# Kernel tuning notes

Measured on AMD Instinct MI355X. Metric: run time of the kernel, lower is better.

The kernel has to match this reference:

```python
import jax, jax.numpy as jnp
import numpy as np

BETA = 0.5  # exp-sum normalization exponent (not a true softmax)


def setup_inputs() -> dict:
    key = jax.random.key(0)
    ks = jax.random.split(key, 12)
    b, h = 1024, 200
    item_num, region_num, user_num = 50000, 1000, 10000
    d, hid = 128, 128  # embed_size == hidden_size (required by the bmm reshape)
    std = 0.01
    return {
        "history": jax.random.randint(ks[0], (1, b, h), 0, item_num),
        "target": jax.random.randint(ks[1], (1, b), 0, item_num),
        "history_region": jax.random.randint(ks[2], (1, b, h), 0, region_num),
        "target_region": jax.random.randint(ks[3], (1, b), 0, region_num),
        "history_visit_rate": jax.random.uniform(ks[4], (1, h), dtype=jnp.float32),
        "dist_mat": jax.random.uniform(ks[5], (b, h), dtype=jnp.float32),
        "uid": 7,
        "embed_target": std * jax.random.normal(ks[6], (item_num, d // 2), dtype=jnp.float32),
        "embed_region": std * jax.random.normal(ks[7], (region_num, d // 2), dtype=jnp.float32),
        "embed_dist": std * jax.random.normal(ks[8], (user_num, region_num), dtype=jnp.float32),
        "Wq": jax.random.normal(ks[9], (hid, d), dtype=jnp.float32) * (1.0 / np.sqrt(d)),
        "Wk": jax.random.normal(ks[10], (hid, d), dtype=jnp.float32) * (1.0 / np.sqrt(d)),
        "Wv": jax.random.normal(ks[11], (d, d), dtype=jnp.float32) * (1.0 / np.sqrt(d)),
    }


def reference(history, target, history_region, target_region, history_visit_rate,
              dist_mat, uid, embed_target, embed_region, embed_dist, Wq, Wk, Wv):
    h_idx = history[0]            # [b, h]
    tgt = target[0]               # [b]
    hr = history_region[0]        # [b, h]
    tr = target_region[0]         # [b]
    hv = history_visit_rate[0]    # [h]
    b, hlen = h_idx.shape

    # embedding gathers + concat (target half | region half)
    hist_emb = jnp.concatenate([embed_target[h_idx], embed_region[hr]], axis=-1)  # [b,h,d]
    tgt_emb = jnp.concatenate([embed_target[tgt], embed_region[tr]], axis=-1)     # [b,d]
    hd = embed_dist[uid][hr]      # [b, h]
    td = embed_dist[uid][tr]      # [b]
    d = tgt_emb.shape[1]

    # QKV projections (torch Linear: y = x @ W.T)
    q = tgt_emb @ Wq.T            # [b, d]  (hidden == d)
    k = hist_emb @ Wk.T           # [b, h, d]
    v = hist_emb @ Wv.T           # [b, h, d]

    # faithful to original: key reshaped (NOT transposed) to [b, d, h]
    k_r = k.reshape(b, d, hlen)
    scores = jnp.einsum('bd,bdh->bh', q, k_r) / jnp.sqrt(jnp.float32(d))  # [b,h]

    # exp / beta-normalized attention with equality mask
    mask = (h_idx != tgt[:, None]).astype(scores.dtype)
    exp_A = jnp.exp(scores) * mask                          # [b,h]
    exp_sum = jnp.sum(exp_A, axis=-1) ** BETA               # [b]
    attn = exp_A / exp_sum[:, None]                         # [b,h]

    # geo weights: td @ hd is a vector-matrix product -> [h], broadcast over b
    geo = jnp.exp(-1.0 / (jax.nn.relu(td @ hd) + 1.0) * dist_mat)  # [b,h]

    result1 = v * (attn + geo)[..., None]                   # [b,h,d]
    result2 = hist_emb * jnp.broadcast_to(hv, (b, hlen))[..., None]
    result = result1 + result2                              # [b,h,d]

    pred = jnp.einsum('bhd,bd->b', result, tgt_emb)         # bmm + sum over h
    return jax.nn.sigmoid(pred)
```

## Files before the change

### kernel.cpp

```cpp
#include <hip/hip_runtime.h>

typedef unsigned short USH;
typedef unsigned int   UIN;

static constexpr int Bn = 1024;
static constexpr int Hn = 200;
static constexpr int Dn = 128;
static constexpr int Dh = 64;
static constexpr int NITEM = 50000;
static constexpr int NREG  = 1000;
static constexpr int MT = 64;
static constexpr int AB_A_BLOCKS = (NITEM + MT - 1) / MT;
static constexpr int AB_B_BLOCKS = (NREG  + MT - 1) / MT;
static constexpr int WTS = 132;
static constexpr int ETS = 69;
static constexpr int CR = 50;

__device__ __forceinline__ float bf2f(USH u) {
  return __uint_as_float(((UIN)u) << 16);
}
__device__ __forceinline__ float2 pb2f2(UIN p) {
  float2 r;
  r.x = __uint_as_float(p << 16);
  r.y = __uint_as_float(p & 0xffff0000u);
  return r;
}
__device__ __forceinline__ USH f2b(float f) {
  UIN x = __float_as_uint(f);
  return (USH)((x + 0x7fffu + ((x >> 16) & 1u)) >> 16);
}
__device__ __forceinline__ UIN addpk(UIN u, UIN v) {
  float2 a = pb2f2(u), b = pb2f2(v);
  return (UIN)f2b(a.x + b.x) | ((UIN)f2b(a.y + b.y) << 16);
}

__global__ __launch_bounds__(256) void g_kernel(
    const int* __restrict__ hregion, const int* __restrict__ tregion,
    const float* __restrict__ embed_dist, const int* __restrict__ uid,
    float* __restrict__ g) {
  int c = threadIdx.x;
  const float* row = embed_dist + (size_t)uid[0] * NREG;
  float acc = 0.f;
  int ibase = blockIdx.x * 16;
  for (int ii = 0; ii < 16; ii++) {
    int i = ibase + ii;
    float td = row[tregion[i]];
    if (c < Hn) acc += td * row[hregion[(size_t)i * Hn + c]];
  }
  if (c < Hn) atomicAdd(&g[c], acc);
}

__global__ __launch_bounds__(256, 2) void ab_kernel(
    const float* __restrict__ Et, const float* __restrict__ Er,
    const float* __restrict__ Wk, USH* __restrict__ A, USH* __restrict__ Bt,
    USH* __restrict__ Ebr, USH* __restrict__ Err, int emit_raw) {
  __shared__ float wt[64 * WTS];
  __shared__ float et[MT * ETS];
  int blk = blockIdx.x, tid = threadIdx.x;
  const float* E; USH* Out; USH* OutR; int nmax, base, koff;
  if (blk < AB_A_BLOCKS) { E = Et; Out = A;  OutR = Ebr; nmax = NITEM; base = blk * MT; koff = 0; }
  else { E = Er; Out = Bt; OutR = Err; nmax = NREG; base = (blk - AB_A_BLOCKS) * MT; koff = 64; }

#pragma unroll
  for (int p = 0; p < 8; p++) {
    int idx = p * 256 + tid;
    int row = idx >> 4, c4 = idx & 15;
    float4 w = *reinterpret_cast<const float4*>(Wk + (size_t)row * Dn + koff + c4 * 4);
    wt[(c4 * 4 + 0) * WTS + row] = w.x;
    wt[(c4 * 4 + 1) * WTS + row] = w.y;
    wt[(c4 * 4 + 2) * WTS + row] = w.z;
    wt[(c4 * 4 + 3) * WTS + row] = w.w;
  }
#pragma unroll
  for (int p = 0; p < 4; p++) {
    int idx = p * 256 + tid;
    int m = idx >> 4, c4 = idx & 15;
    int gi = base + m;
    float4 e = make_float4(0.f, 0.f, 0.f, 0.f);
    if (gi < nmax) e = *reinterpret_cast<const float4*>(E + (size_t)gi * Dh + c4 * 4);
    et[m * ETS + c4 * 4 + 0] = e.x;
    et[m * ETS + c4 * 4 + 1] = e.y;
    et[m * ETS + c4 * 4 + 2] = e.z;
    et[m * ETS + c4 * 4 + 3] = e.w;
  }
  __syncthreads();

  if (emit_raw) {
#pragma unroll
    for (int q = 0; q < 8; q++) {
      int idx = q * 256 + tid;
      int m = idx >> 5, kp = idx & 31;
      int gi = base + m;
      if (gi < nmax) {
        UIN pk = (UIN)f2b(et[m * ETS + 2 * kp]) | ((UIN)f2b(et[m * ETS + 2 * kp + 1]) << 16);
        *reinterpret_cast<UIN*>(OutR + (size_t)gi * Dh + 2 * kp) = pk;
      }
    }
  }

  int jt = tid & 15, it = tid >> 4;
  const float* wb = wt + jt * 8;
  const float* eb = et + (it * 4) * ETS;
  float c[4][8];
#pragma unroll
  for (int ii = 0; ii < 4; ii++)
#pragma unroll
    for (int jj = 0; jj < 8; jj++) c[ii][jj] = 0.f;

#pragma unroll 2
  for (int k = 0; k < 64; k++) {
    float4 w0 = *reinterpret_cast<const float4*>(wb + (size_t)k * WTS);
    float4 w1 = *reinterpret_cast<const float4*>(wb + (size_t)k * WTS + 4);
    float e0 = eb[k], e1 = eb[ETS + k], e2 = eb[2 * ETS + k], e3 = eb[3 * ETS + k];
    c[0][0] += e0 * w0.x; c[0][1] += e0 * w0.y; c[0][2] += e0 * w0.z; c[0][3] += e0 * w0.w;
    c[0][4] += e0 * w1.x; c[0][5] += e0 * w1.y; c[0][6] += e0 * w1.z; c[0][7] += e0 * w1.w;
    c[1][0] += e1 * w0.x; c[1][1] += e1 * w0.y; c[1][2] += e1 * w0.z; c[1][3] += e1 * w0.w;
    c[1][4] += e1 * w1.x; c[1][5] += e1 * w1.y; c[1][6] += e1 * w1.z; c[1][7] += e1 * w1.w;
    c[2][0] += e2 * w0.x; c[2][1] += e2 * w0.y; c[2][2] += e2 * w0.z; c[2][3] += e2 * w0.w;
    c[2][4] += e2 * w1.x; c[2][5] += e2 * w1.y; c[2][6] += e2 * w1.z; c[2][7] += e2 * w1.w;
    c[3][0] += e3 * w0.x; c[3][1] += e3 * w0.y; c[3][2] += e3 * w0.z; c[3][3] += e3 * w0.w;
    c[3][4] += e3 * w1.x; c[3][5] += e3 * w1.y; c[3][6] += e3 * w1.z; c[3][7] += e3 * w1.w;
  }

#pragma unroll
  for (int ii = 0; ii < 4; ii++) {
    int item = base + it * 4 + ii;
    if (item < nmax) {
      uint4 pk;
      pk.x = (UIN)f2b(c[ii][0]) | ((UIN)f2b(c[ii][1]) << 16);
      pk.y = (UIN)f2b(c[ii][2]) | ((UIN)f2b(c[ii][3]) << 16);
      pk.z = (UIN)f2b(c[ii][4]) | ((UIN)f2b(c[ii][5]) << 16);
      pk.w = (UIN)f2b(c[ii][6]) | ((UIN)f2b(c[ii][7]) << 16);
      *reinterpret_cast<uint4*>(Out + (size_t)item * Dn + jt * 8) = pk;
    }
  }
}

__global__ __launch_bounds__(256, 4) void sc_kernel(
    const int* __restrict__ history, const int* __restrict__ target,
    const int* __restrict__ hregion, const int* __restrict__ tregion,
    const float* __restrict__ Et, const float* __restrict__ Er,
    const float* __restrict__ Wq, const USH* __restrict__ A,
    const USH* __restrict__ Bt, float* __restrict__ psc) {
  __shared__ USH kvs[CR * Dn];
  __shared__ float tgtE[128], qp[128], qv[32];
  int b = blockIdx.x, i = b >> 2, h = b & 3;
  int tid = threadIdx.x;
  const int* hrow = history + (size_t)i * Hn + CR * h;
  const int* rrow = hregion + (size_t)i * Hn + CR * h;

  if (tid < 64)       tgtE[tid] = Et[(size_t)target[i] * Dh + tid];
  else if (tid < 128) tgtE[tid] = Er[(size_t)tregion[i] * Dh + (tid - 64)];

  int rlane = tid & 15, rgrp = tid >> 4;
#pragma unroll
  for (int p = 0; p < 4; p++) {
    int t = p * 16 + rgrp;
    if (t < CR) {
      int ia = hrow[t], ib = rrow[t];
      uint4 av = *reinterpret_cast<const uint4*>(A  + (size_t)ia * Dn + rlane * 8);
      uint4 bv = *reinterpret_cast<const uint4*>(Bt + (size_t)ib * Dn + rlane * 8);
      uint4 pk;
      pk.x = addpk(av.x, bv.x); pk.y = addpk(av.y, bv.y);
      pk.z = addpk(av.z, bv.z); pk.w = addpk(av.w, bv.w);
      *reinterpret_cast<uint4*>(&kvs[t * Dn + rlane * 8]) = pk;
    }
  }
  __syncthreads();

  if (tid < 128) {
    int ql = tid >> 2, quarter = tid & 3;
    int a = 32 * h + ql;
    const float4* wp = reinterpret_cast<const float4*>(Wq + (size_t)a * Dn + quarter * 32);
    float acc = 0.f;
#pragma unroll
    for (int k4 = 0; k4 < 8; k4++) {
      float4 w = wp[k4];
      const float* tv = &tgtE[quarter * 32 + k4 * 4];
      acc += w.x * tv[0] + w.y * tv[1] + w.z * tv[2] + w.w * tv[3];
    }
    qp[tid] = acc;
  }
  __syncthreads();
  if (tid < 32)
    qv[tid] = (qp[4 * tid] + qp[4 * tid + 1] + qp[4 * tid + 2] + qp[4 * tid + 3])
              * 0.088388347648318447f;
  __syncthreads();

  if (tid < Hn) {
    float acc = 0.f;
    const USH* kp = &kvs[tid];
#pragma unroll
    for (int a = 0; a < 32; a++) acc += qv[a] * bf2f(kp[a * 200]);
    psc[((size_t)i * 4 + h) * Hn + tid] = acc;
  }
}

__global__ __launch_bounds__(256, 4) void ep_kernel(
    const int* __restrict__ history, const int* __restrict__ target,
    const int* __restrict__ hregion, const int* __restrict__ tregion,
    const float* __restrict__ hv, const float* __restrict__ dist_mat,
    const float* __restrict__ Et, const float* __restrict__ Er,
    const float* __restrict__ Wv, const float* __restrict__ g,
    const USH* __restrict__ Ebr, const USH* __restrict__ Err,
    const float* __restrict__ psc, int use_raw, float* __restrict__ out) {
  __shared__ float tgtE[128], uv[128], red[8];
  int i = blockIdx.x, tid = threadIdx.x, lane = tid & 63, wave = tid >> 6;
  int tgt_i = target[i], tr_i = tregion[i];
  const int* hrow = history + (size_t)i * Hn;
  const int* rrow = hregion + (size_t)i * Hn;

  if (tid < 64)       tgtE[tid] = Et[(size_t)tgt_i * Dh + tid];
  else if (tid < 128) tgtE[tid] = Er[(size_t)tr_i * Dh + (tid - 64)];
  __syncthreads();

  if (tid >= 128) {
    int d = tid - 128;
    float a0 = 0.f, a1 = 0.f, a2 = 0.f, a3 = 0.f;
#pragma unroll 8
    for (int j = 0; j < 128; j += 4) {
      a0 += Wv[(size_t)(j + 0) * Dn + d] * tgtE[j + 0];
      a1 += Wv[(size_t)(j + 1) * Dn + d] * tgtE[j + 1];
      a2 += Wv[(size_t)(j + 2) * Dn + d] * tgtE[j + 2];
      a3 += Wv[(size_t)(j + 3) * Dn + d] * tgtE[j + 3];
    }
    uv[d] = (a0 + a1) + (a2 + a3);
  }
  __syncthreads();

  float ea = 0.f, sc1 = 0.f, sc2 = 0.f;
  if (tid < Hn) {
    const float* pp = psc + (size_t)i * 4 * Hn + tid;
    float s = (pp[0] + pp[Hn]) + (pp[2 * Hn] + pp[3 * Hn]);
    int ia2 = hrow[tid], ib2 = rrow[tid];
    float p1 = 0.f, p2 = 0.f;
    if (use_raw) {
      const uint4* epu = reinterpret_cast<const uint4*>(Ebr + (size_t)ia2 * Dh);
      const uint4* rpu = reinterpret_cast<const uint4*>(Err + (size_t)ib2 * Dh);
#pragma unroll
      for (int k8 = 0; k8 < 8; k8++) {
        uint4 e = epu[k8], r = rpu[k8];
        float2 e0 = pb2f2(e.x), e1 = pb2f2(e.y), e2 = pb2f2(e.z), e3 = pb2f2(e.w);
        float2 r0 = pb2f2(r.x), r1 = pb2f2(r.y), r2 = pb2f2(r.z), r3 = pb2f2(r.w);
        const float* u0 = &uv[k8 * 8];       const float* t0 = &tgtE[k8 * 8];
        const float* u1 = &uv[64 + k8 * 8];  const float* t1 = &tgtE[64 + k8 * 8];
        p1 += e0.x * u0[0] + e0.y * u0[1] + e1.x * u0[2] + e1.y * u0[3]
            + e2.x * u0[4] + e2.y * u0[5] + e3.x * u0[6] + e3.y * u0[7]
            + r0.x * u1[0] + r0.y * u1[1] + r1.x * u1[2] + r1.y * u1[3]
            + r2.x * u1[4] + r2.y * u1[5] + r3.x * u1[6] + r3.y * u1[7];
        p2 += e0.x * t0[0] + e0.y * t0[1] + e1.x * t0[2] + e1.y * t0[3]
            + e2.x * t0[4] + e2.y * t0[5] + e3.x * t0[6] + e3.y * t0[7]
            + r0.x * t1[0] + r0.y * t1[1] + r1.x * t1[2] + r1.y * t1[3]
            + r2.x * t1[4] + r2.y * t1[5] + r3.x * t1[6] + r3.y * t1[7];
      }
    } else {
      const float4* ep = reinterpret_cast<const float4*>(Et + (size_t)ia2 * Dh);
      const float4* rp = reinterpret_cast<const float4*>(Er + (size_t)ib2 * Dh);
#pragma unroll
      for (int k4 = 0; k4 < 16; k4++) {
        float4 e = ep[k4], r = rp[k4];
        const float* u0 = &uv[k4 * 4];        const float* t0 = &tgtE[k4 * 4];
        const float* u1 = &uv[64 + k4 * 4];   const float* t1 = &tgtE[64 + k4 * 4];
        p1 += e.x * u0[0] + e.y * u0[1] + e.z * u0[2] + e.w * u0[3]
            + r.x * u1[0] + r.y * u1[1] + r.z * u1[2] + r.w * u1[3];
        p2 += e.x * t0[0] + e.y * t0[1] + e.z * t0[2] + e.w * t0[3]
            + r.x * t1[0] + r.y * t1[1] + r.z * t1[2] + r.w * t1[3];
      }
    }
    sc1 = p1; sc2 = p2;
    ea = (ia2 != tgt_i) ? __expf(s) : 0.f;
  }

  float wsum = ea;
  for (int off = 32; off > 0; off >>= 1) wsum += __shfl_down(wsum, off, 64);
  if (lane == 0) red[wave] = wsum;
  __syncthreads();
  float esum = red[0] + red[1] + red[2] + red[3];
  float inv = esum > 0.f ? 1.f / sqrtf(esum) : 0.f;

  float part = 0.f;
  if (tid < Hn) {
    float attn = ea * inv;
    float gc = g[tid]; gc = gc > 0.f ? gc : 0.f;
    float dm = dist_mat[(size_t)i * Hn + tid];
    float geo = __expf(-dm / (gc + 1.f));
    part = (attn + geo) * sc1 + hv[tid] * sc2;
  }
  __syncthreads();
  for (int off = 32; off > 0; off >>= 1) part += __shfl_down(part, off, 64);
  if (lane == 0) red[wave] = part;
  __syncthreads();
  if (tid == 0) {
    float pred = red[0] + red[1] + red[2] + red[3];
    out[i] = 1.f / (1.f + __expf(-pred));
  }
}

extern "C" void kernel_launch(void* const* d_in, const int* in_sizes, int n_in,
                              void* d_out, int out_size, void* d_ws, size_t ws_size,
                              hipStream_t stream) {
  const int*   history = (const int*)d_in[0];
  const int*   target  = (const int*)d_in[1];
  const int*   hregion = (const int*)d_in[2];
  const int*   tregion = (const int*)d_in[3];
  const float* hv      = (const float*)d_in[4];
  const float* dist    = (const float*)d_in[5];
  const int*   uid     = (const int*)d_in[6];
  const float* Et      = (const float*)d_in[7];
  const float* Er      = (const float*)d_in[8];
  const float* Edist   = (const float*)d_in[9];
  const float* Wq      = (const float*)d_in[10];
  const float* Wk      = (const float*)d_in[11];
  const float* Wv      = (const float*)d_in[12];

  float* g = (float*)d_ws;
  USH* A   = (USH*)((char*)d_ws + 1024);
  USH* Bt  = A + (size_t)NITEM * Dn;
  USH* Ebr = Bt + (size_t)NREG * Dn;
  USH* Err = Ebr + (size_t)NITEM * Dh;
  float* psc = (float*)(Err + (size_t)NREG * Dh);
  size_t need_raw = 1024 + 2 * ((size_t)NITEM * Dn + (size_t)NREG * Dn +
                                (size_t)NITEM * Dh + (size_t)NREG * Dh) +
                    4 * (size_t)Bn * 4 * Hn;
  int use_raw = (ws_size >= need_raw) ? 1 : 0;
  float* out = (float*)d_out;

  hipMemsetAsync(g, 0, Hn * sizeof(float), stream);
  g_kernel<<<Bn / 16, 256, 0, stream>>>(hregion, tregion, Edist, uid, g);
  ab_kernel<<<AB_A_BLOCKS + AB_B_BLOCKS, 256, 0, stream>>>(Et, Er, Wk, A, Bt,
                                                           Ebr, Err, use_raw);
  sc_kernel<<<Bn * 4, 256, 0, stream>>>(history, target, hregion, tregion,
                                        Et, Er, Wq, A, Bt, psc);
  ep_kernel<<<Bn, 256, 0, stream>>>(history, target, hregion, tregion, hv, dist,
                                    Et, Er, Wv, g, Ebr, Err, psc, use_raw, out);
}
```

Measured before the change: 172.7 us.

## Interleave projected and raw embeddings, precompute q/u vectors, move dot products into sc_kernel

Projected-key rows and raw bf16 embeddings are stored interleaved in a single 192-wide row per item, so sc_kernel's gathers hit adjacent memory. The per-batch Wq and Wv target projections move into extra blocks of ab_kernel and are written to global memory, so they are no longer recomputed in every sc and ep block. The history-embedding dot products against u and the target embedding move from ep_kernel into sc_kernel, reusing the same gathered rows and leaving ep_kernel as a light reduction. This costs more workspace, extra global round-trips for qvt, uvt and s12, and drops the fp32 fallback path when the workspace is small.

Measured after the change: 160.2 us. 7.3% less time.

```diff
diff --git a/kernel.cpp b/kernel.cpp
--- a/kernel.cpp
+++ b/kernel.cpp
@@ -12,9 +12,12 @@
 static constexpr int MT = 64;
 static constexpr int AB_A_BLOCKS = (NITEM + MT - 1) / MT;
 static constexpr int AB_B_BLOCKS = (NREG  + MT - 1) / MT;
+static constexpr int AB_TOT = AB_A_BLOCKS + AB_B_BLOCKS;
+static constexpr int QU_BLOCKS = Bn / 4;
 static constexpr int WTS = 132;
 static constexpr int ETS = 69;
-static constexpr int CR = 50;
+static constexpr int CR  = 50;
+static constexpr int AFS = 192;
 
 __device__ __forceinline__ float bf2f(USH u) {
   return __uint_as_float(((UIN)u) << 16);
@@ -52,14 +55,61 @@
 
 __global__ __launch_bounds__(256, 2) void ab_kernel(
     const float* __restrict__ Et, const float* __restrict__ Er,
-    const float* __restrict__ Wk, USH* __restrict__ A, USH* __restrict__ Bt,
-    USH* __restrict__ Ebr, USH* __restrict__ Err, int emit_raw) {
+    const float* __restrict__ Wk, const float* __restrict__ Wq,
+    const float* __restrict__ Wv, const int* __restrict__ target,
+    const int* __restrict__ tregion,
+    USH* __restrict__ Af, USH* __restrict__ Bf,
+    float* __restrict__ qvt, float* __restrict__ uvt) {
   __shared__ float wt[64 * WTS];
   __shared__ float et[MT * ETS];
   int blk = blockIdx.x, tid = threadIdx.x;
-  const float* E; USH* Out; USH* OutR; int nmax, base, koff;
-  if (blk < AB_A_BLOCKS) { E = Et; Out = A;  OutR = Ebr; nmax = NITEM; base = blk * MT; koff = 0; }
-  else { E = Er; Out = Bt; OutR = Err; nmax = NREG; base = (blk - AB_A_BLOCKS) * MT; koff = 64; }
+
+  if (blk >= AB_TOT) {
+    float* te = wt;
+    int i0 = (blk - AB_TOT) * 4;
+#pragma unroll
+    for (int v = 0; v < 2; v++) {
+      int idx = v * 256 + tid;
+      int ii = idx >> 7, d = idx & 127;
+      int it = i0 + ii;
+      te[ii * 128 + d] = (d < 64) ? Et[(size_t)target[it] * Dh + d]
+                                  : Er[(size_t)tregion[it] * Dh + (d - 64)];
+    }
+    __syncthreads();
+    int j = tid & 127, half = tid >> 7;
+    float a0 = 0.f, a1 = 0.f, a2 = 0.f, a3 = 0.f;
+    if (half == 0) {
+      const float* wr = Wq + (size_t)j * Dn;
+#pragma unroll 8
+      for (int k = 0; k < 128; k++) {
+        float w = wr[k];
+        a0 += w * te[k]; a1 += w * te[128 + k];
+        a2 += w * te[256 + k]; a3 += w * te[384 + k];
+      }
+      const float s = 0.088388347648318447f;
+      qvt[(size_t)(i0 + 0) * Dn + j] = a0 * s;
+      qvt[(size_t)(i0 + 1) * Dn + j] = a1 * s;
+      qvt[(size_t)(i0 + 2) * Dn + j] = a2 * s;
+      qvt[(size_t)(i0 + 3) * Dn + j] = a3 * s;
+    } else {
+      int d = j;
+#pragma unroll 8
+      for (int k = 0; k < 128; k++) {
+        float w = Wv[(size_t)k * Dn + d];
+        a0 += w * te[k]; a1 += w * te[128 + k];
+        a2 += w * te[256 + k]; a3 += w * te[384 + k];
+      }
+      uvt[(size_t)(i0 + 0) * Dn + d] = a0;
+      uvt[(size_t)(i0 + 1) * Dn + d] = a1;
+      uvt[(size_t)(i0 + 2) * Dn + d] = a2;
+      uvt[(size_t)(i0 + 3) * Dn + d] = a3;
+    }
+    return;
+  }
+
+  const float* E; USH* Out; int nmax, base, koff;
+  if (blk < AB_A_BLOCKS) { E = Et; Out = Af; nmax = NITEM; base = blk * MT; koff = 0; }
+  else { E = Er; Out = Bf; nmax = NREG; base = (blk - AB_A_BLOCKS) * MT; koff = 64; }
 
 #pragma unroll
   for (int p = 0; p < 8; p++) {
@@ -85,16 +135,14 @@
   }
   __syncthreads();
 
-  if (emit_raw) {
-#pragma unroll
-    for (int q = 0; q < 8; q++) {
-      int idx = q * 256 + tid;
-      int m = idx >> 5, kp = idx & 31;
-      int gi = base + m;
-      if (gi < nmax) {
-        UIN pk = (UIN)f2b(et[m * ETS + 2 * kp]) | ((UIN)f2b(et[m * ETS + 2 * kp + 1]) << 16);
-        *reinterpret_cast<UIN*>(OutR + (size_t)gi * Dh + 2 * kp) = pk;
-      }
+#pragma unroll
+  for (int q = 0; q < 8; q++) {
+    int idx = q * 256 + tid;
+    int m = idx >> 5, kp = idx & 31;
+    int gi = base + m;
+    if (gi < nmax) {
+      UIN pk = (UIN)f2b(et[m * ETS + 2 * kp]) | ((UIN)f2b(et[m * ETS + 2 * kp + 1]) << 16);
+      *reinterpret_cast<UIN*>(Out + (size_t)gi * AFS + 128 + 2 * kp) = pk;
     }
   }
 
@@ -131,7 +179,7 @@
       pk.y = (UIN)f2b(c[ii][2]) | ((UIN)f2b(c[ii][3]) << 16);
       pk.z = (UIN)f2b(c[ii][4]) | ((UIN)f2b(c[ii][5]) << 16);
       pk.w = (UIN)f2b(c[ii][6]) | ((UIN)f2b(c[ii][7]) << 16);
-      *reinterpret_cast<uint4*>(Out + (size_t)item * Dn + jt * 8) = pk;
+      *reinterpret_cast<uint4*>(Out + (size_t)item * AFS + jt * 8) = pk;
     }
   }
 }
@@ -140,52 +188,70 @@
     const int* __restrict__ history, const int* __restrict__ target,
     const int* __restrict__ hregion, const int* __restrict__ tregion,
     const float* __restrict__ Et, const float* __restrict__ Er,
-    const float* __restrict__ Wq, const USH* __restrict__ A,
-    const USH* __restrict__ Bt, float* __restrict__ psc) {
+    const float* __restrict__ qvt, const float* __restrict__ uvt,
+    const USH* __restrict__ Af, const USH* __restrict__ Bf,
+    float* __restrict__ psc, float2* __restrict__ s12) {
   __shared__ USH kvs[CR * Dn];
-  __shared__ float tgtE[128], qp[128], qv[32];
+  __shared__ float tgtE[128], uvf[128], qv[32];
   int b = blockIdx.x, i = b >> 2, h = b & 3;
   int tid = threadIdx.x;
   const int* hrow = history + (size_t)i * Hn + CR * h;
   const int* rrow = hregion + (size_t)i * Hn + CR * h;
 
-  if (tid < 64)       tgtE[tid] = Et[(size_t)target[i] * Dh + tid];
-  else if (tid < 128) tgtE[tid] = Er[(size_t)tregion[i] * Dh + (tid - 64)];
-
-  int rlane = tid & 15, rgrp = tid >> 4;
-#pragma unroll
-  for (int p = 0; p < 4; p++) {
-    int t = p * 16 + rgrp;
-    if (t < CR) {
-      int ia = hrow[t], ib = rrow[t];
-      uint4 av = *reinterpret_cast<const uint4*>(A  + (size_t)ia * Dn + rlane * 8);
-      uint4 bv = *reinterpret_cast<const uint4*>(Bt + (size_t)ib * Dn + rlane * 8);
-      uint4 pk;
-      pk.x = addpk(av.x, bv.x); pk.y = addpk(av.y, bv.y);
-      pk.z = addpk(av.z, bv.z); pk.w = addpk(av.w, bv.w);
-      *reinterpret_cast<uint4*>(&kvs[t * Dn + rlane * 8]) = pk;
-    }
-  }
-  __syncthreads();
-
   if (tid < 128) {
-    int ql = tid >> 2, quarter = tid & 3;
-    int a = 32 * h + ql;
-    const float4* wp = reinterpret_cast<const float4*>(Wq + (size_t)a * Dn + quarter * 32);
-    float acc = 0.f;
-#pragma unroll
-    for (int k4 = 0; k4 < 8; k4++) {
-      float4 w = wp[k4];
-      const float* tv = &tgtE[quarter * 32 + k4 * 4];
-      acc += w.x * tv[0] + w.y * tv[1] + w.z * tv[2] + w.w * tv[3];
-    }
-    qp[tid] = acc;
-  }
-  __syncthreads();
-  if (tid < 32)
-    qv[tid] = (qp[4 * tid] + qp[4 * tid + 1] + qp[4 * tid + 2] + qp[4 * tid + 3])
-              * 0.088388347648318447f;
-  __syncthreads();
+    tgtE[tid] = (tid < 64) ? Et[(size_t)target[i] * Dh + tid]
+                           : Er[(size_t)tregion[i] * Dh + (tid - 64)];
+  } else {
+    uvf[tid - 128] = uvt[(size_t)i * Dn + (tid - 128)];
+  }
+  if (tid < 32) qv[tid] = qvt[(size_t)i * Dn + 32 * h + tid];
+
+  {
+    int rlane = tid & 15, rgrp = tid >> 4;
+#pragma unroll
+    for (int p = 0; p < 4; p++) {
+      int t = p * 16 + rgrp;
+      if (t < CR) {
+        int ia = hrow[t], ib = rrow[t];
+        uint4 av = *reinterpret_cast<const uint4*>(Af + (size_t)ia * AFS + rlane * 8);
+        uint4 bv = *reinterpret_cast<const uint4*>(Bf + (size_t)ib * AFS + rlane * 8);
+        uint4 pk;
+        pk.x = addpk(av.x, bv.x); pk.y = addpk(av.y, bv.y);
+        pk.z = addpk(av.z, bv.z); pk.w = addpk(av.w, bv.w);
+        *reinterpret_cast<uint4*>(&kvs[t * Dn + rlane * 8]) = pk;
+      }
+    }
+  }
+  __syncthreads();
+
+  {
+    int l8 = tid & 7, r8 = tid >> 3;
+#pragma unroll
+    for (int p = 0; p < 2; p++) {
+      int t = p * 32 + r8;
+      if (t < CR) {
+        int ia = hrow[t], ib = rrow[t];
+        uint4 e = *reinterpret_cast<const uint4*>(Af + (size_t)ia * AFS + 128 + l8 * 8);
+        uint4 r = *reinterpret_cast<const uint4*>(Bf + (size_t)ib * AFS + 128 + l8 * 8);
+        float2 e0 = pb2f2(e.x), e1 = pb2f2(e.y), e2 = pb2f2(e.z), e3 = pb2f2(e.w);
+        float2 r0 = pb2f2(r.x), r1 = pb2f2(r.y), r2 = pb2f2(r.z), r3 = pb2f2(r.w);
+        const float* u0 = &uvf[l8 * 8];       const float* t0 = &tgtE[l8 * 8];
+        const float* u1 = &uvf[64 + l8 * 8];  const float* t1 = &tgtE[64 + l8 * 8];
+        float s1a = e0.x * u0[0] + e0.y * u0[1] + e1.x * u0[2] + e1.y * u0[3]
+                  + e2.x * u0[4] + e2.y * u0[5] + e3.x * u0[6] + e3.y * u0[7]
+                  + r0.x * u1[0] + r0.y * u1[1] + r1.x * u1[2] + r1.y * u1[3]
+                  + r2.x * u1[4] + r2.y * u1[5] + r3.x * u1[6] + r3.y * u1[7];
+        float s2a = e0.x * t0[0] + e0.y * t0[1] + e1.x * t0[2] + e1.y * t0[3]
+                  + e2.x * t0[4] + e2.y * t0[5] + e3.x * t0[6] + e3.y * t0[7]
+                  + r0.x * t1[0] + r0.y * t1[1] + r1.x * t1[2] + r1.y * t1[3]
+                  + r2.x * t1[4] + r2.y * t1[5] + r3.x * t1[6] + r3.y * t1[7];
+        s1a += __shfl_xor(s1a, 1, 64); s2a += __shfl_xor(s2a, 1, 64);
+        s1a += __shfl_xor(s1a, 2, 64); s2a += __shfl_xor(s2a, 2, 64);
+        s1a += __shfl_xor(s1a, 4, 64); s2a += __shfl_xor(s2a, 4, 64);
+        if (l8 == 0) s12[(size_t)i * Hn + CR * h + t] = make_float2(s1a, s2a);
+      }
+    }
+  }
 
   if (tid < Hn) {
     float acc = 0.f;
@@ -196,81 +262,22 @@
   }
 }
 
-__global__ __launch_bounds__(256, 4) void ep_kernel(
+__global__ __launch_bounds__(256, 8) void ep_kernel(
     const int* __restrict__ history, const int* __restrict__ target,
-    const int* __restrict__ hregion, const int* __restrict__ tregion,
     const float* __restrict__ hv, const float* __restrict__ dist_mat,
-    const float* __restrict__ Et, const float* __restrict__ Er,
-    const float* __restrict__ Wv, const float* __restrict__ g,
-    const USH* __restrict__ Ebr, const USH* __restrict__ Err,
-    const float* __restrict__ psc, int use_raw, float* __restrict__ out) {
-  __shared__ float tgtE[128], uv[128], red[8];
+    const float* __restrict__ g, const float* __restrict__ psc,
+    const float2* __restrict__ s12, float* __restrict__ out) {
+  __shared__ float red[8];
   int i = blockIdx.x, tid = threadIdx.x, lane = tid & 63, wave = tid >> 6;
-  int tgt_i = target[i], tr_i = tregion[i];
-  const int* hrow = history + (size_t)i * Hn;
-  const int* rrow = hregion + (size_t)i * Hn;
-
-  if (tid < 64)       tgtE[tid] = Et[(size_t)tgt_i * Dh + tid];
-  else if (tid < 128) tgtE[tid] = Er[(size_t)tr_i * Dh + (tid - 64)];
-  __syncthreads();
-
-  if (tid >= 128) {
-    int d = tid - 128;
-    float a0 = 0.f, a1 = 0.f, a2 = 0.f, a3 = 0.f;
-#pragma unroll 8
-    for (int j = 0; j < 128; j += 4) {
-      a0 += Wv[(size_t)(j + 0) * Dn + d] * tgtE[j + 0];
-      a1 += Wv[(size_t)(j + 1) * Dn + d] * tgtE[j + 1];
-      a2 += Wv[(size_t)(j + 2) * Dn + d] * tgtE[j + 2];
-      a3 += Wv[(size_t)(j + 3) * Dn + d] * tgtE[j + 3];
-    }
-    uv[d] = (a0 + a1) + (a2 + a3);
-  }
-  __syncthreads();
-
-  float ea = 0.f, sc1 = 0.f, sc2 = 0.f;
+  int tgt_i = target[i];
+
+  float ea = 0.f; float2 sv = make_float2(0.f, 0.f);
   if (tid < Hn) {
     const float* pp = psc + (size_t)i * 4 * Hn + tid;
     float s = (pp[0] + pp[Hn]) + (pp[2 * Hn] + pp[3 * Hn]);
-    int ia2 = hrow[tid], ib2 = rrow[tid];
-    float p1 = 0.f, p2 = 0.f;
-    if (use_raw) {
-      const uint4* epu = reinterpret_cast<const uint4*>(Ebr + (size_t)ia2 * Dh);
-      const uint4* rpu = reinterpret_cast<const uint4*>(Err + (size_t)ib2 * Dh);
-#pragma unroll
-      for (int k8 = 0; k8 < 8; k8++) {
-        uint4 e = epu[k8], r = rpu[k8];
-        float2 e0 = pb2f2(e.x), e1 = pb2f2(e.y), e2 = pb2f2(e.z), e3 = pb2f2(e.w);
-        float2 r0 = pb2f2(r.x), r1 = pb2f2(r.y), r2 = pb2f2(r.z), r3 = pb2f2(r.w);
-        const float* u0 = &uv[k8 * 8];       const float* t0 = &tgtE[k8 * 8];
-        const float* u1 = &uv[64 + k8 * 8];  const float* t1 = &tgtE[64 + k8 * 8];
-        p1 += e0.x * u0[0] + e0.y * u0[1] + e1.x * u0[2] + e1.y * u0[3]
-            + e2.x * u0[4] + e2.y * u0[5] + e3.x * u0[6] + e3.y * u0[7]
-            + r0.x * u1[0] + r0.y * u1[1] + r1.x * u1[2] + r1.y * u1[3]
-            + r2.x * u1[4] + r2.y * u1[5] + r3.x * u1[6] + r3.y * u1[7];
-        p2 += e0.x * t0[0] + e0.y * t0[1] + e1.x * t0[2] + e1.y * t0[3]
-            + e2.x * t0[4] + e2.y * t0[5] + e3.x * t0[6] + e3.y * t0[7]
-            + r0.x * t1[0] + r0.y * t1[1] + r1.x * t1[2] + r1.y * t1[3]
-            + r2.x * t1[4] + r2.y * t1[5] + r3.x * t1[6] + r3.y * t1[7];
-      }
-    } else {
-      const float4* ep = reinterpret_cast<const float4*>(Et + (size_t)ia2 * Dh);
-      const float4* rp = reinterpret_cast<const float4*>(Er + (size_t)ib2 * Dh);
-#pragma unroll
-      for (int k4 = 0; k4 < 16; k4++) {
-        float4 e = ep[k4], r = rp[k4];
-        const float* u0 = &uv[k4 * 4];        const float* t0 = &tgtE[k4 * 4];
-        const float* u1 = &uv[64 + k4 * 4];   const float* t1 = &tgtE[64 + k4 * 4];
-        p1 += e.x * u0[0] + e.y * u0[1] + e.z * u0[2] + e.w * u0[3]
-            + r.x * u1[0] + r.y * u1[1] + r.z * u1[2] + r.w * u1[3];
-        p2 += e.x * t0[0] + e.y * t0[1] + e.z * t0[2] + e.w * t0[3]
-            + r.x * t1[0] + r.y * t1[1] + r.z * t1[2] + r.w * t1[3];
-      }
-    }
-    sc1 = p1; sc2 = p2;
-    ea = (ia2 != tgt_i) ? __expf(s) : 0.f;
-  }
-
+    sv = s12[(size_t)i * Hn + tid];
+    ea = (history[(size_t)i * Hn + tid] != tgt_i) ? __expf(s) : 0.f;
+  }
   float wsum = ea;
   for (int off = 32; off > 0; off >>= 1) wsum += __shfl_down(wsum, off, 64);
   if (lane == 0) red[wave] = wsum;
@@ -280,11 +287,10 @@
 
   float part = 0.f;
   if (tid < Hn) {
-    float attn = ea * inv;
     float gc = g[tid]; gc = gc > 0.f ? gc : 0.f;
     float dm = dist_mat[(size_t)i * Hn + tid];
     float geo = __expf(-dm / (gc + 1.f));
-    part = (attn + geo) * sc1 + hv[tid] * sc2;
+    part = (ea * inv + geo) * sv.x + hv[tid] * sv.y;
   }
   __syncthreads();
   for (int off = 32; off > 0; off >>= 1) part += __shfl_down(part, off, 64);
@@ -313,24 +319,21 @@
   const float* Wk      = (const float*)d_in[11];
   const float* Wv      = (const float*)d_in[12];
 
-  float* g = (float*)d_ws;
-  USH* A   = (USH*)((char*)d_ws + 1024);
-  USH* Bt  = A + (size_t)NITEM * Dn;
-  USH* Ebr = Bt + (size_t)NREG * Dn;
-  USH* Err = Ebr + (size_t)NITEM * Dh;
-  float* psc = (float*)(Err + (size_t)NREG * Dh);
-  size_t need_raw = 1024 + 2 * ((size_t)NITEM * Dn + (size_t)NREG * Dn +
-                                (size_t)NITEM * Dh + (size_t)NREG * Dh) +
-                    4 * (size_t)Bn * 4 * Hn;
-  int use_raw = (ws_size >= need_raw) ? 1 : 0;
+  char* w = (char*)d_ws;
+  float* g   = (float*)w;
+  USH*   Af  = (USH*)(w + 1024);
+  USH*   Bf  = Af + (size_t)NITEM * AFS;
+  float* qvt = (float*)(Bf + (size_t)NREG * AFS);
+  float* uvt = qvt + (size_t)Bn * Dn;
+  float* psc = uvt + (size_t)Bn * Dn;
+  float2* s12 = (float2*)(psc + (size_t)Bn * 4 * Hn);
   float* out = (float*)d_out;
 
   hipMemsetAsync(g, 0, Hn * sizeof(float), stream);
   g_kernel<<<Bn / 16, 256, 0, stream>>>(hregion, tregion, Edist, uid, g);
-  ab_kernel<<<AB_A_BLOCKS + AB_B_BLOCKS, 256, 0, stream>>>(Et, Er, Wk, A, Bt,
-                                                           Ebr, Err, use_raw);
+  ab_kernel<<<AB_TOT + QU_BLOCKS, 256, 0, stream>>>(Et, Er, Wk, Wq, Wv, target,
+                                                    tregion, Af, Bf, qvt, uvt);
   sc_kernel<<<Bn * 4, 256, 0, stream>>>(history, target, hregion, tregion,
-                                        Et, Er, Wq, A, Bt, psc);
-  ep_kernel<<<Bn, 256, 0, stream>>>(history, target, hregion, tregion, hv, dist,
-                                    Et, Er, Wv, g, Ebr, Err, psc, use_raw, out);
-}
+                                        Et, Er, qvt, uvt, Af, Bf, psc, s12);
+  ep_kernel<<<Bn, 256, 0, stream>>>(history, target, hv, dist, g, psc, s12, out);
+}
```
